# Kernel tuning notes

Hardware: AMD Instinct MI355X
Metric: run time of the kernel (lower is better)

The kernel has to match this reference:

```python
import jax, jax.numpy as jnp
import numpy as np

N_HEAD = 12
EPS = 1e-6


def setup_inputs() -> dict:
    key = jax.random.key(0)
    k1, k2, k3 = jax.random.split(key, 3)
    B, T, C = 2, 2048, 768
    x = jax.random.normal(k1, (B, T, C), dtype=jnp.float32)
    c_attn_w = jax.random.normal(k2, (3 * C, C), dtype=jnp.float32) * 0.02
    c_proj_w = jax.random.normal(k3, (C, C), dtype=jnp.float32) * 0.02
    temperature = jnp.ones((1,), dtype=jnp.float32) * np.sqrt(C // N_HEAD)
    return {"x": x, "c_attn_w": c_attn_w, "c_proj_w": c_proj_w, "temperature": temperature}


def reference(x, c_attn_w, c_proj_w, temperature):
    B, T, C = x.shape
    H = N_HEAD
    D = C // H
    qkv = x @ c_attn_w.T  # [B,T,3C] (no bias)
    q, k, v = jnp.split(qkv, 3, axis=2)
    # [B,H,T,D]
    q = q.reshape(B, T, H, D).transpose(0, 2, 1, 3)
    k = k.reshape(B, T, H, D).transpose(0, 2, 1, 3)
    v = v.reshape(B, T, H, D).transpose(0, 2, 1, 3)

    # autocorrelation via FFT along time axis, zero-padded to 2T
    fft_len = 2 * T
    q_fft = jnp.fft.rfft(q, n=fft_len, axis=2)
    k_fft = jnp.fft.rfft(k, n=fft_len, axis=2)
    corr = jnp.fft.irfft(q_fft * jnp.conj(k_fft), n=fft_len, axis=2)[:, :, :T, :]
    corr_weights = corr.mean(axis=-1) / (temperature + EPS)  # [B,H,T] over lag

    # causal lag mask: position t may use lags 0..t
    t_idx = jnp.arange(T)
    lag_mask = t_idx[None, :] <= t_idx[:, None]  # [T(pos), T(lag)]
    weights_masked = jnp.where(lag_mask[None, None], corr_weights[:, :, None, :], -jnp.inf)
    attn = jax.nn.softmax(weights_masked, axis=-1)  # [B,H,T,T] over lags
    attn = jnp.nan_to_num(attn)

    # Original gathers v at source position s = clamp(t - lag, 0), producing a
    # (B,H,T,T,D) tensor. Since lags > t have zero weight, this is exactly
    # y[t] = sum_{s<=t} attn[t, t-s] * v[s]. Build the position-score matrix by
    # gathering attn along the lag axis — avoids the 5D blowup, same math.
    lag_idx = jnp.clip(t_idx[:, None] - t_idx[None, :], 0)  # [T(pos), T(src)]
    scores = jnp.take_along_axis(attn, lag_idx[None, None], axis=-1)
    scores = jnp.where(lag_mask[None, None], scores, 0.0)  # zero out s > t
    y = jnp.einsum('bhts,bhsd->bhtd', scores, v)

    y = y.transpose(0, 2, 1, 3).reshape(B, T, C)
    return y @ c_proj_w.T
```

## Files before the change

kernel.cpp:

```cpp
#include <hip/hip_runtime.h>

#define T_ 2048
#define B_ 2
#define H_ 12
#define C_ 768
#define M_ 4096
#define BH_ (B_ * H_)
#define RSTR 2200

typedef __attribute__((ext_vector_type(4))) float f32x4;
typedef __attribute__((ext_vector_type(16))) float f32x16;
typedef __attribute__((ext_vector_type(8))) __bf16 bf16x8;
typedef __attribute__((ext_vector_type(4))) __bf16 bf16x4;

#define GLOAD16(GP, LP)                                                   \
  __builtin_amdgcn_global_load_lds(                                       \
      (__attribute__((address_space(1))) void*)(GP),                      \
      (__attribute__((address_space(3))) void*)(LP), 16, 0, 0)


__global__ __launch_bounds__(256) void cvt3_k(const float* __restrict__ x,
                                              const float* __restrict__ ca,
                                              const float* __restrict__ cp,
                                              __bf16* __restrict__ xb,
                                              __bf16* __restrict__ wb,
                                              __bf16* __restrict__ pb) {
  const int id = blockIdx.x;
  const float* src;
  __bf16* dst;
  size_t base;
  if (id < 1536) { src = x; dst = xb; base = (size_t)id * 2048; }
  else if (id < 2400) { src = ca; dst = wb; base = (size_t)(id - 1536) * 2048; }
  else { src = cp; dst = pb; base = (size_t)(id - 2400) * 2048; }
  const size_t o = base + (size_t)threadIdx.x * 8;
  f32x4 v0 = *(const f32x4*)(src + o);
  f32x4 v1 = *(const f32x4*)(src + o + 4);
  bf16x8 r;
#pragma unroll
  for (int j = 0; j < 4; ++j) { r[j] = (__bf16)v0[j]; r[4 + j] = (__bf16)v1[j]; }
  *(bf16x8*)(dst + o) = r;
}

__global__ __launch_bounds__(256) void gemm_qkv(const __bf16* __restrict__ A,
                                                const __bf16* __restrict__ Bm,
                                                __bf16* __restrict__ Qp,
                                                __bf16* __restrict__ Kp,
                                                __bf16* __restrict__ Vp) {
  __shared__ __align__(16) __bf16 sA[4096];
  __shared__ __align__(16) __bf16 sB[4096];
  const int tid = threadIdx.x;
  const int id = blockIdx.x;
  const int lg = (id & 7) * 72 + (id >> 3);
  const int m0 = (lg / 18) * 128, n0 = (lg % 18) * 128;
  const bool isV = (n0 >= 1536);
  const int lane = tid & 63, w = tid >> 6;
  const int wr = w >> 1, wc = w & 1;
  const int fr = lane & 15;
  const int ko = (lane >> 4) << 3;
  const int srow = lane >> 2, scol = (lane & 3) << 3;
  const __bf16* Ab = A + (size_t)(m0 + srow) * 768 + scol;
  const __bf16* Bb = Bm + (size_t)(n0 + srow) * 768 + scol;
  const int c0 = 2 * w, c1 = 2 * w + 1;
  f32x4 acc[4][4] = {};

  if (isV) {
    for (int k0 = 0; k0 < 768; k0 += 32) {
      GLOAD16(Ab + (size_t)c0 * 16 * 768 + k0, &sA[c0 * 512]);
      GLOAD16(Ab + (size_t)c1 * 16 * 768 + k0, &sA[c1 * 512]);
      GLOAD16(Bb + (size_t)c0 * 16 * 768 + k0, &sB[c0 * 512]);
      GLOAD16(Bb + (size_t)c1 * 16 * 768 + k0, &sB[c1 * 512]);
      __syncthreads();
      bf16x8 a[4], b[4];
#pragma unroll
      for (int m = 0; m < 4; ++m) a[m] = *(const bf16x8*)&sA[(wr * 64 + m * 16 + fr) * 32 + ko];
#pragma unroll
      for (int n = 0; n < 4; ++n) b[n] = *(const bf16x8*)&sB[(wc * 64 + n * 16 + fr) * 32 + ko];
#pragma unroll
      for (int m = 0; m < 4; ++m)
#pragma unroll
        for (int n = 0; n < 4; ++n)
          acc[m][n] = __builtin_amdgcn_mfma_f32_16x16x32_bf16(a[m], b[n], acc[m][n], 0, 0, 0);
      __syncthreads();
    }
    const int orow = (lane >> 4) << 2, ocol = lane & 15;
#pragma unroll
    for (int m = 0; m < 4; ++m)
#pragma unroll
      for (int n = 0; n < 4; ++n) {
        int r = m0 + wr * 64 + m * 16 + orow;
        int c = n0 + wc * 64 + n * 16 + ocol;
        int hd = c - 1536;
        int h = hd >> 6, d = hd & 63;
        int b = r >> 11, t = r & 2047;
        int bh = b * H_ + h;
        int chunk = t >> 6, sk = t & 63;
        int kc = sk >> 4, hf = (sk >> 3) & 1, j0 = sk & 7;
        bf16x4 pk;
#pragma unroll
        for (int j = 0; j < 4; ++j) pk[j] = (__bf16)acc[m][n][j];
        *(bf16x4*)(Vp + ((size_t)bh * 32 + chunk) * 4096 + (d >> 5) * 2048 +
                   kc * 512 + (hf * 32 + (d & 31)) * 8 + j0) = pk;
      }
  } else {
    for (int k0 = 0; k0 < 768; k0 += 32) {
      GLOAD16(Ab + (size_t)c0 * 16 * 768 + k0, &sA[c0 * 512]);
      GLOAD16(Ab + (size_t)c1 * 16 * 768 + k0, &sA[c1 * 512]);
      GLOAD16(Bb + (size_t)c0 * 16 * 768 + k0, &sB[c0 * 512]);
      GLOAD16(Bb + (size_t)c1 * 16 * 768 + k0, &sB[c1 * 512]);
      __syncthreads();
      bf16x8 a[4], b[4];
#pragma unroll
      for (int m = 0; m < 4; ++m) a[m] = *(const bf16x8*)&sA[(wr * 64 + m * 16 + fr) * 32 + ko];
#pragma unroll
      for (int n = 0; n < 4; ++n) b[n] = *(const bf16x8*)&sB[(wc * 64 + n * 16 + fr) * 32 + ko];
#pragma unroll
      for (int m = 0; m < 4; ++m)
#pragma unroll
        for (int n = 0; n < 4; ++n)
          acc[m][n] = __builtin_amdgcn_mfma_f32_16x16x32_bf16(b[n], a[m], acc[m][n], 0, 0, 0);
      __syncthreads();
    }
    const int tcol = lane & 15, dbase = (lane >> 4) << 2;
#pragma unroll
    for (int m = 0; m < 4; ++m)
#pragma unroll
      for (int n = 0; n < 4; ++n) {
        int t4 = m0 + wr * 64 + m * 16 + tcol;
        int c = n0 + wc * 64 + n * 16 + dbase;
        int sec = c / 768;
        int hd = c - sec * 768;
        int h = hd >> 6, d = hd & 63;
        int b = t4 >> 11, t = t4 & 2047;
        int bh = b * H_ + h;
        int tile = t >> 5, rr = t & 31;
        int kc = d >> 4, half = (d >> 3) & 1, dj = d & 7;
        bf16x4 pk;
#pragma unroll
        for (int j = 0; j < 4; ++j) pk[j] = (__bf16)acc[m][n][j];
        *(bf16x4*)((sec == 0 ? Qp : Kp) + ((size_t)bh * 64 + tile) * 2048 +
                   kc * 512 + (half * 32 + rr) * 8 + dj) = pk;
      }
  }
}

__global__ __launch_bounds__(256) void gemm_out(const __bf16* __restrict__ A,
                                                const __bf16* __restrict__ Bm,
                                                float* __restrict__ C) {
  __shared__ __align__(16) __bf16 sA[2048];
  __shared__ __align__(16) __bf16 sB[2048];
  const int tid = threadIdx.x;
  const int id = blockIdx.x;
  const int lg = (id & 7) * 96 + (id >> 3);
  const int m0 = (lg / 12) * 64, n0 = (lg % 12) * 64;
  const int lane = tid & 63, w = tid >> 6;
  const int wr = w >> 1, wc = w & 1;
  const int fr = lane & 15;
  const int ko = (lane >> 4) << 3;
  const int srow = tid >> 2, scol = (tid & 3) << 3;
  const __bf16* Ab = A + (size_t)(m0 + srow) * 768 + scol;
  const __bf16* Bb = Bm + (size_t)(n0 + srow) * 768 + scol;
  f32x4 acc[2][2] = {};
  for (int k0 = 0; k0 < 768; k0 += 32) {
    GLOAD16(Ab + k0, &sA[w * 512]);
    GLOAD16(Bb + k0, &sB[w * 512]);
    __syncthreads();
    bf16x8 a[2], b[2];
#pragma unroll
    for (int m = 0; m < 2; ++m) a[m] = *(const bf16x8*)&sA[(wr * 32 + m * 16 + fr) * 32 + ko];
#pragma unroll
    for (int n = 0; n < 2; ++n) b[n] = *(const bf16x8*)&sB[(wc * 32 + n * 16 + fr) * 32 + ko];
#pragma unroll
    for (int m = 0; m < 2; ++m)
#pragma unroll
      for (int n = 0; n < 2; ++n)
        acc[m][n] = __builtin_amdgcn_mfma_f32_16x16x32_bf16(a[m], b[n], acc[m][n], 0, 0, 0);
    __syncthreads();
  }
  const int orow = (lane >> 4) << 2, ocol = lane & 15;
#pragma unroll
  for (int m = 0; m < 2; ++m)
#pragma unroll
    for (int n = 0; n < 2; ++n) {
      int r = m0 + wr * 32 + m * 16 + orow;
      int c = n0 + wc * 32 + n * 16 + ocol;
#pragma unroll
      for (int j = 0; j < 4; ++j) C[(size_t)(r + j) * 768 + c] = acc[m][n][j];
    }
}

__global__ __launch_bounds__(256) void corr_k2(const __bf16* __restrict__ Qp,
                                               const __bf16* __restrict__ Kp,
                                               float* __restrict__ P36) {
  __shared__ float tile[4][1056];
  __shared__ float prow[4][288];
  const int tid = threadIdx.x;
  int id = blockIdx.x;
  int sub = id >> 3;
  const int bh = (id & 7) * 3 + sub / 36;
  const int pi = sub % 36;
  int x = pi, qb = 0;
  while (x >= 8 - qb) { x -= 8 - qb; ++qb; }
  const int tc = qb + x;
  const int lane = tid & 63, w = tid >> 6;

  for (int i = tid; i < 4 * 288; i += 256) ((float*)prow)[i] = 0.f;

  const __bf16* qp = Qp + ((size_t)bh << 17) + (lane << 3);
  const __bf16* kp = Kp + ((size_t)bh << 17) + (lane << 3);
  const int qA = 8 * qb + 2 * w;
  f32x16 acc0 = {}, acc1 = {};
  const bf16x8 zf = {};
  bf16x8 Af[2][4], Kc[2][4], Kpv[4];

  {
    const int t0 = 8 * tc;
#pragma unroll
    for (int kc = 0; kc < 4; ++kc) Af[0][kc] = *(const bf16x8*)(qp + t0 * 2048 + kc * 512);
    const int s0 = t0 - qA, sm = s0 - 1;
#pragma unroll
    for (int kc = 0; kc < 4; ++kc) {
      Kc[0][kc] = (s0 >= 0) ? *(const bf16x8*)(kp + s0 * 2048 + kc * 512) : zf;
      Kpv[kc] = (sm >= 0) ? *(const bf16x8*)(kp + sm * 2048 + kc * 512) : zf;
    }
  }
#pragma unroll
  for (int ii = 0; ii < 8; ++ii) {
    const int cur = ii & 1, nxt = cur ^ 1;
    if (ii < 7) {
      const int tn = 8 * tc + ii + 1;
      const int sn = tn - qA;
#pragma unroll
      for (int kc = 0; kc < 4; ++kc) {
        Af[nxt][kc] = *(const bf16x8*)(qp + tn * 2048 + kc * 512);
        Kc[nxt][kc] = (sn >= 0) ? *(const bf16x8*)(kp + sn * 2048 + kc * 512) : zf;
      }
    }
#pragma unroll
    for (int kc = 0; kc < 4; ++kc) {
      acc0 = __builtin_amdgcn_mfma_f32_32x32x16_bf16(Af[cur][kc], Kc[cur][kc], acc0, 0, 0, 0);
      acc1 = __builtin_amdgcn_mfma_f32_32x32x16_bf16(Af[cur][kc], Kpv[kc], acc1, 0, 0, 0);
    }
#pragma unroll
    for (int kc = 0; kc < 4; ++kc) Kpv[kc] = Kc[cur][kc];
  }

  const int col = lane & 31, hi = lane >> 5;
  const int d = lane - 31;
  __syncthreads();
#pragma unroll
  for (int b01 = 0; b01 < 2; ++b01) {
    const f32x16* ac = (b01 == 0) ? &acc0 : &acc1;
#pragma unroll
    for (int j = 0; j < 16; ++j) {
      int row = (j & 3) + ((j >> 2) << 3) + 4 * hi;
      tile[w][row * 33 + col] = (*ac)[j];
    }
    __syncthreads();
    if (lane < 63) {
      float s = 0.f;
#pragma unroll
      for (int c = 0; c < 32; ++c) {
        int r = c + d;
        bool ok = (unsigned)r < 32u;
        float val = tile[w][(ok ? r : 0) * 33 + c];
        s += ok ? val : 0.f;
      }
      prow[w][32 * (2 * w + b01) + d + 32] += s;
    }
    __syncthreads();
  }

  float* Pd = P36 + ((size_t)pi * BH_ + bh) * T_;
  float ov[8];
#pragma unroll
  for (int u = 0; u < 8; ++u) {
    int L = (tid << 3) + u;
    int l = L - 256 * qb;
    float s = 0.f;
    if (l >= -31 && l < 256)
      s = prow[0][l + 32] + prow[1][l + 32] + prow[2][l + 32] + prow[3][l + 32];
    ov[u] = s;
  }
  *(f32x4*)(Pd + (tid << 3)) = *(f32x4*)&ov[0];
  *(f32x4*)(Pd + (tid << 3) + 4) = *(f32x4*)&ov[4];
}

__global__ __launch_bounds__(256) void soft_k(const float* __restrict__ P,
                                              const float* __restrict__ temp,
                                              __bf16* __restrict__ Rb,
                                              float* __restrict__ zinv) {
  __shared__ float se[T_];
  __shared__ float lm[4], wsum[4];
  const int bh = blockIdx.x, tid = threadIdx.x;
  const int lane = tid & 63, wid = tid >> 6;
  const float scale = 1.0f / (64.0f * (temp[0] + 1e-6f));
  f32x4 sa = {}, sb = {};
#pragma unroll
  for (int j = 0; j < 36; ++j) {
    const float* pp = P + ((size_t)j * BH_ + bh) * T_ + (tid << 3);
    sa += *(const f32x4*)pp;
    sb += *(const f32x4*)(pp + 4);
  }
  float v[8];
#pragma unroll
  for (int i = 0; i < 4; ++i) { v[i] = sa[i] * scale; v[4 + i] = sb[i] * scale; }
  float m = v[0];
#pragma unroll
  for (int i = 1; i < 8; ++i) m = fmaxf(m, v[i]);
#pragma unroll
  for (int off = 1; off < 64; off <<= 1) m = fmaxf(m, __shfl_xor(m, off));
  if (lane == 0) lm[wid] = m;
  __syncthreads();
  m = fmaxf(fmaxf(lm[0], lm[1]), fmaxf(lm[2], lm[3]));
  float ex[8], pr[8], run = 0;
#pragma unroll
  for (int i = 0; i < 8; ++i) { ex[i] = __expf(v[i] - m); run += ex[i]; pr[i] = run; }
  float s = run;
  for (int off = 1; off < 64; off <<= 1) {
    float o = __shfl_up(s, off);
    if (lane >= off) s += o;
  }
  if (lane == 63) wsum[wid] = s;
  __syncthreads();
  float base = s - run;
  for (int jw = 0; jw < wid; ++jw) base += wsum[jw];
#pragma unroll
  for (int i = 0; i < 8; ++i) {
    int t = (tid << 3) + i;
    zinv[(size_t)bh * T_ + t] = 1.0f / (base + pr[i]);
    se[t] = ex[i];
  }
  __syncthreads();
  __bf16* rb = Rb + (size_t)bh * 8 * RSTR;
  for (int c = tid; c < RSTR / 8; c += 256) {
    int i0 = c << 3;
#pragma unroll
    for (int p = 0; p < 8; ++p) {
      bf16x8 ovv;
#pragma unroll
      for (int e = 0; e < 8; ++e) {
        int idx = T_ - 1 - p - (i0 + e);
        ovv[e] = (__bf16)((idx >= 0) ? se[idx] : 0.f);
      }
      *(bf16x8*)(rb + p * RSTR + i0) = ovv;
    }
  }
}

__global__ __launch_bounds__(256) void conv_k(const __bf16* __restrict__ Vp,
                                              const __bf16* __restrict__ Rb,
                                              const float* __restrict__ zinv,
                                              __bf16* __restrict__ y2b) {
  __shared__ __align__(16) __bf16 revc[8 * RSTR];
  const int tid = threadIdx.x;
  int id = blockIdx.x;
  int sub = id >> 3;
  const int bh = (id & 7) * 3 + (sub >> 4);
  const int pr = sub & 15;
  const int lane = tid & 63, w = tid >> 6;

  const __bf16* rb = Rb + (size_t)bh * 8 * RSTR;
  for (int c = tid; c < RSTR; c += 256)
    *(bf16x8*)&revc[c << 3] = *(const bf16x8*)(rb + ((size_t)c << 3));
  __syncthreads();

  const int fr = lane & 31, kg = (lane >> 5) << 3;
  const int tt = (w < 2) ? (64 * pr + 32 * w) : (64 * (31 - pr) + 32 * (w - 2));
  const int trow = tt + fr;
  const int pp = (T_ - 1 - trow) & 7;
  const int obase = (T_ - 1 - trow) - pp;
  const __bf16* vpb = Vp + (size_t)bh * 131072 + (lane << 3);
  f32x16 acc0 = {}, acc1 = {};
  const int nst = (tt >> 6) + 1;

  bf16x8 A00, A01, A02, A03, A10, A11, A12, A13;
  bf16x8 B00, B01, B02, B03, B10, B11, B12, B13;
  bf16x8 C00, C01, C02, C03, C10, C11, C12, C13;

#define LOADV(P, CH)                                                          \
  {                                                                           \
    const __bf16* vb_ = vpb + (size_t)(CH) * 4096;                            \
    P##00 = *(const bf16x8*)(vb_);          P##01 = *(const bf16x8*)(vb_ + 512);  \
    P##02 = *(const bf16x8*)(vb_ + 1024);   P##03 = *(const bf16x8*)(vb_ + 1536); \
    P##10 = *(const bf16x8*)(vb_ + 2048);   P##11 = *(const bf16x8*)(vb_ + 2560); \
    P##12 = *(const bf16x8*)(vb_ + 3072);   P##13 = *(const bf16x8*)(vb_ + 3584); \
  }
#define MSTEP(P, ST)                                                          \
  {                                                                           \
    const int ab_ = pp * RSTR + obase + (ST) * 64 + kg;                       \
    bf16x8 a0_ = *(const bf16x8*)&revc[ab_];                                  \
    bf16x8 a1_ = *(const bf16x8*)&revc[ab_ + 16];                             \
    bf16x8 a2_ = *(const bf16x8*)&revc[ab_ + 32];                             \
    bf16x8 a3_ = *(const bf16x8*)&revc[ab_ + 48];                             \
    acc0 = __builtin_amdgcn_mfma_f32_32x32x16_bf16(a0_, P##00, acc0, 0, 0, 0);\
    acc1 = __builtin_amdgcn_mfma_f32_32x32x16_bf16(a0_, P##10, acc1, 0, 0, 0);\
    acc0 = __builtin_amdgcn_mfma_f32_32x32x16_bf16(a1_, P##01, acc0, 0, 0, 0);\
    acc1 = __builtin_amdgcn_mfma_f32_32x32x16_bf16(a1_, P##11, acc1, 0, 0, 0);\
    acc0 = __builtin_amdgcn_mfma_f32_32x32x16_bf16(a2_, P##02, acc0, 0, 0, 0);\
    acc1 = __builtin_amdgcn_mfma_f32_32x32x16_bf16(a2_, P##12, acc1, 0, 0, 0);\
    acc0 = __builtin_amdgcn_mfma_f32_32x32x16_bf16(a3_, P##03, acc0, 0, 0, 0);\
    acc1 = __builtin_amdgcn_mfma_f32_32x32x16_bf16(a3_, P##13, acc1, 0, 0, 0);\
  }

  LOADV(A, 0);
  if (nst > 1) LOADV(B, 1);
  if (nst > 2) LOADV(C, 2);
  int st = 0;
  while (true) {
    MSTEP(A, st); if (st + 3 < nst) LOADV(A, st + 3); if (++st >= nst) break;
    MSTEP(B, st); if (st + 3 < nst) LOADV(B, st + 3); if (++st >= nst) break;
    MSTEP(C, st); if (st + 3 < nst) LOADV(C, st + 3); if (++st >= nst) break;
  }
#undef LOADV
#undef MSTEP

  const int b = bh / H_, h = bh % H_;
  const int ocol = lane & 31, rbj = (lane >> 5) << 2;
  const float* zp = zinv + (size_t)bh * T_;
#pragma unroll
  for (int j = 0; j < 16; ++j) {
    int row = (j & 3) + ((j >> 2) << 3) + rbj;
    int t = tt + row;
    float zi = zp[t];
    __bf16* yr = y2b + ((size_t)b * T_ + t) * C_ + h * 64;
    yr[ocol] = (__bf16)(acc0[j] * zi);
    yr[32 + ocol] = (__bf16)(acc1[j] * zi);
  }
}

extern "C" void kernel_launch(void* const* d_in, const int* in_sizes, int n_in,
                              void* d_out, int out_size, void* d_ws, size_t ws_size,
                              hipStream_t stream) {
  const float* x = (const float*)d_in[0];
  const float* c_attn = (const float*)d_in[1];
  const float* c_proj = (const float*)d_in[2];
  const float* temp = (const float*)d_in[3];
  float* out = (float*)d_out;

  __bf16* Qp = (__bf16*)d_ws;
  __bf16* Kp = Qp + (size_t)3145728;
  __bf16* Vp = Kp + (size_t)3145728;
  __bf16* Rb = Vp + (size_t)3145728;
  float* zinv = (float*)(Rb + 422400);
  float* P36 = zinv + 49152;
  __bf16* pb = (__bf16*)(P36 + 1769472);
  __bf16* xb = pb + 589824;
  __bf16* wb = xb + 3145728;
  __bf16* y2b = xb;

  cvt3_k<<<dim3(2688), 256, 0, stream>>>(x, c_attn, c_proj, xb, wb, pb);
  gemm_qkv<<<dim3(576), 256, 0, stream>>>(xb, wb, Qp, Kp, Vp);
  corr_k2<<<dim3(864), 256, 0, stream>>>(Qp, Kp, P36);
  soft_k<<<dim3(BH_), 256, 0, stream>>>(P36, temp, Rb, zinv);
  conv_k<<<dim3(384), 256, 0, stream>>>(Vp, Rb, zinv, y2b);
  gemm_out<<<dim3(768), 256, 0, stream>>>(y2b, pb, out);
}
```

Measured before the change: 91.62 us.

## Stage Q and K rows in LDS ring buffer for correlation kernel

The correlation kernel now loads Q rows and K rows into shared memory with async global-to-LDS loads, keeping a 9-slot ring buffer of K rows. Each K row is then shared by all four waves instead of every wave reloading overlapping K rows from global memory. MFMAs for out-of-range lags are skipped through branches rather than fed zero fragments. In exchange it adds two block barriers per time step and serialises load then compute, which removes the old register double-buffered prefetch overlap.

```diff
diff --git a/kernel.cpp b/kernel.cpp
--- a/kernel.cpp
+++ b/kernel.cpp
@@ -188,11 +188,12 @@
     }
 }
 
-__global__ __launch_bounds__(256) void corr_k2(const __bf16* __restrict__ Qp,
+__global__ __launch_bounds__(256) void corr_k3(const __bf16* __restrict__ Qp,
                                                const __bf16* __restrict__ Kp,
                                                float* __restrict__ P36) {
-  __shared__ float tile[4][1056];
-  __shared__ float prow[4][288];
+  __shared__ __align__(16) char smem[40960];
+  __bf16* sQ = (__bf16*)smem;
+  __bf16* sK = (__bf16*)(smem + 4096);
   const int tid = threadIdx.x;
   int id = blockIdx.x;
   int sub = id >> 3;
@@ -203,57 +204,63 @@
   const int tc = qb + x;
   const int lane = tid & 63, w = tid >> 6;
 
-  for (int i = tid; i < 4 * 288; i += 256) ((float*)prow)[i] = 0.f;
-
-  const __bf16* qp = Qp + ((size_t)bh << 17) + (lane << 3);
-  const __bf16* kp = Kp + ((size_t)bh << 17) + (lane << 3);
+  const __bf16* qbase = Qp + ((size_t)bh << 17);
+  const __bf16* kbase = Kp + ((size_t)bh << 17);
+  const int wq = w << 9;
+
+  const int smin = 8 * (tc - qb) - 8;
+#pragma unroll
+  for (int li = 0; li < 8; ++li) {
+    int si = smin + li;
+    if (si >= 0) GLOAD16(kbase + (size_t)si * 2048 + tid * 8, sK + li * 2048 + wq);
+  }
+
+  int r0 = 8 - 2 * w;
+  int r1 = 7 - 2 * w;
+  int ss = 8;
   const int qA = 8 * qb + 2 * w;
   f32x16 acc0 = {}, acc1 = {};
-  const bf16x8 zf = {};
-  bf16x8 Af[2][4], Kc[2][4], Kpv[4];
-
-  {
-    const int t0 = 8 * tc;
-#pragma unroll
-    for (int kc = 0; kc < 4; ++kc) Af[0][kc] = *(const bf16x8*)(qp + t0 * 2048 + kc * 512);
-    const int s0 = t0 - qA, sm = s0 - 1;
-#pragma unroll
-    for (int kc = 0; kc < 4; ++kc) {
-      Kc[0][kc] = (s0 >= 0) ? *(const bf16x8*)(kp + s0 * 2048 + kc * 512) : zf;
-      Kpv[kc] = (sm >= 0) ? *(const bf16x8*)(kp + sm * 2048 + kc * 512) : zf;
-    }
-  }
-#pragma unroll
-  for (int ii = 0; ii < 8; ++ii) {
-    const int cur = ii & 1, nxt = cur ^ 1;
-    if (ii < 7) {
-      const int tn = 8 * tc + ii + 1;
-      const int sn = tn - qA;
-#pragma unroll
-      for (int kc = 0; kc < 4; ++kc) {
-        Af[nxt][kc] = *(const bf16x8*)(qp + tn * 2048 + kc * 512);
-        Kc[nxt][kc] = (sn >= 0) ? *(const bf16x8*)(kp + sn * 2048 + kc * 512) : zf;
-      }
-    }
-#pragma unroll
-    for (int kc = 0; kc < 4; ++kc) {
-      acc0 = __builtin_amdgcn_mfma_f32_32x32x16_bf16(Af[cur][kc], Kc[cur][kc], acc0, 0, 0, 0);
-      acc1 = __builtin_amdgcn_mfma_f32_32x32x16_bf16(Af[cur][kc], Kpv[kc], acc1, 0, 0, 0);
-    }
-#pragma unroll
-    for (int kc = 0; kc < 4; ++kc) Kpv[kc] = Kc[cur][kc];
-  }
-
+
+  for (int tau = 0; tau < 8; ++tau) {
+    const int ti = 8 * tc + tau;
+    GLOAD16(qbase + (size_t)ti * 2048 + tid * 8, sQ + wq);
+    GLOAD16(kbase + (size_t)(ti - 8 * qb) * 2048 + tid * 8, sK + ss * 2048 + wq);
+    __syncthreads();
+    bf16x8 qv[4];
+    const __bf16* qf = sQ + lane * 8;
+#pragma unroll
+    for (int kc = 0; kc < 4; ++kc) qv[kc] = *(const bf16x8*)(qf + kc * 512);
+    const int si0 = ti - qA;
+    if (si0 >= 0) {
+      const __bf16* kf = sK + r0 * 2048 + lane * 8;
+#pragma unroll
+      for (int kc = 0; kc < 4; ++kc)
+        acc0 = __builtin_amdgcn_mfma_f32_32x32x16_bf16(qv[kc], *(const bf16x8*)(kf + kc * 512), acc0, 0, 0, 0);
+    }
+    if (si0 - 1 >= 0) {
+      const __bf16* kf = sK + r1 * 2048 + lane * 8;
+#pragma unroll
+      for (int kc = 0; kc < 4; ++kc)
+        acc1 = __builtin_amdgcn_mfma_f32_32x32x16_bf16(qv[kc], *(const bf16x8*)(kf + kc * 512), acc1, 0, 0, 0);
+    }
+    __syncthreads();
+    if (++r0 == 9) r0 = 0;
+    if (++r1 == 9) r1 = 0;
+    if (++ss == 9) ss = 0;
+  }
+
+  float* tile = (float*)smem;
+  float* prow = (float*)(smem + 16896);
+  for (int i = tid; i < 1152; i += 256) prow[i] = 0.f;
   const int col = lane & 31, hi = lane >> 5;
   const int d = lane - 31;
-  __syncthreads();
 #pragma unroll
   for (int b01 = 0; b01 < 2; ++b01) {
     const f32x16* ac = (b01 == 0) ? &acc0 : &acc1;
 #pragma unroll
     for (int j = 0; j < 16; ++j) {
       int row = (j & 3) + ((j >> 2) << 3) + 4 * hi;
-      tile[w][row * 33 + col] = (*ac)[j];
+      tile[w * 1056 + row * 33 + col] = (*ac)[j];
     }
     __syncthreads();
     if (lane < 63) {
@@ -262,10 +269,10 @@
       for (int c = 0; c < 32; ++c) {
         int r = c + d;
         bool ok = (unsigned)r < 32u;
-        float val = tile[w][(ok ? r : 0) * 33 + c];
+        float val = tile[w * 1056 + (ok ? r : 0) * 33 + c];
         s += ok ? val : 0.f;
       }
-      prow[w][32 * (2 * w + b01) + d + 32] += s;
+      prow[w * 288 + 32 * (2 * w + b01) + d + 32] += s;
     }
     __syncthreads();
   }
@@ -278,7 +285,7 @@
     int l = L - 256 * qb;
     float s = 0.f;
     if (l >= -31 && l < 256)
-      s = prow[0][l + 32] + prow[1][l + 32] + prow[2][l + 32] + prow[3][l + 32];
+      s = prow[l + 32] + prow[288 + l + 32] + prow[576 + l + 32] + prow[864 + l + 32];
     ov[u] = s;
   }
   *(f32x4*)(Pd + (tid << 3)) = *(f32x4*)&ov[0];
@@ -450,7 +457,7 @@
 
   cvt3_k<<<dim3(2688), 256, 0, stream>>>(x, c_attn, c_proj, xb, wb, pb);
   gemm_qkv<<<dim3(576), 256, 0, stream>>>(xb, wb, Qp, Kp, Vp);
-  corr_k2<<<dim3(864), 256, 0, stream>>>(Qp, Kp, P36);
+  corr_k3<<<dim3(864), 256, 0, stream>>>(Qp, Kp, P36);
   soft_k<<<dim3(BH_), 256, 0, stream>>>(P36, temp, Rb, zinv);
   conv_k<<<dim3(384), 256, 0, stream>>>(Vp, Rb, zinv, y2b);
   gemm_out<<<dim3(768), 256, 0, stream>>>(y2b, pb, out);
```

After: 91.37 us (median of 2 runs). No clear change (-0.3%).
